# Optimization experiments

Measured on AMD Instinct MI355X. Metric: run time of the kernel, lower is better.

The kernel has to match this reference:

```python
import jax, jax.numpy as jnp
import numpy as np

C = 256          # in_channels
CI = 128         # inter_channels = C // reduction
N_B, H, W = 4, 64, 64


def setup_inputs() -> dict:
    key = jax.random.key(0)
    ks = jax.random.split(key, 9)
    std = 0.01
    inp = {
        "x": jax.random.normal(ks[0], (N_B, C, H, W), dtype=jnp.float32),
        # 1x1 conv weights stored as [out_ch, in_ch]
        "w_g": jax.random.normal(ks[1], (CI, C), dtype=jnp.float32) * std,
        "b_g": jnp.zeros((CI,), dtype=jnp.float32),
        "w_theta": jax.random.normal(ks[2], (CI, C), dtype=jnp.float32) * std,
        "b_theta": jnp.zeros((CI,), dtype=jnp.float32),
        "w_phi": jax.random.normal(ks[3], (CI, C), dtype=jnp.float32) * std,
        "b_phi": jnp.zeros((CI,), dtype=jnp.float32),
        # conv_out: use small random instead of exact zeros so output is non-trivial
        "w_out": jax.random.normal(ks[4], (C, CI), dtype=jnp.float32) * std,
        "b_out": jnp.zeros((C,), dtype=jnp.float32),
    }
    return inp


def reference(x, w_g, b_g, w_theta, b_theta, w_phi, b_phi, w_out, b_out):
    n, c, h, w = x.shape
    nhw = h * w
    xf = x.reshape(n, c, nhw)                                   # [n, C, N]
    # 1x1 convs == channel matmuls
    g_x = jnp.einsum('ncs,oc->nso', xf, w_g) + b_g              # [n, N, CI]
    theta_x = jnp.einsum('ncs,oc->nso', xf, w_theta) + b_theta  # [n, N, CI]
    phi_x = jnp.einsum('ncs,oc->nos', xf, w_phi) + b_phi[None, :, None]  # [n, CI, N]
    # pairwise weights: [n, N, N]
    pw = jnp.einsum('nqc,ncs->nqs', theta_x, phi_x)
    # faithful to original: DIVIDE by d**-0.5 (i.e. multiply by sqrt(d))
    pw = pw / (theta_x.shape[-1] ** (-0.5))
    pw = jax.nn.softmax(pw, axis=-1)
    y = jnp.einsum('nqs,nsc->nqc', pw, g_x)                     # [n, N, CI]
    y = y.transpose(0, 2, 1).reshape(n, -1, h, w)               # [n, CI, H, W]
    out = jnp.einsum('nchw,oc->nohw', y, w_out) + b_out[None, :, None, None]
    return x + out
```

## Files before the change

### kernel.cpp

```cpp
#include <hip/hip_runtime.h>
#include <cmath>

typedef __attribute__((ext_vector_type(8))) short bf16x8;
typedef __attribute__((ext_vector_type(4))) float f32x4;
typedef __attribute__((ext_vector_type(16))) float f32x16;

#define MFMA16(a,b,c)  __builtin_amdgcn_mfma_f32_16x16x32_bf16((a),(b),(c),0,0,0)
#define MFMA32(a,b,c)  __builtin_amdgcn_mfma_f32_32x32x16_bf16((a),(b),(c),0,0,0)

#if __has_builtin(__builtin_amdgcn_exp2f)
#define EXP2F(x) __builtin_amdgcn_exp2f(x)
#else
#define EXP2F(x) exp2f(x)
#endif

#define KSCALE 16.3222312f

#define NB 4
#define CH 256
#define CI 128
#define NS 4096

__device__ __forceinline__ unsigned short f2bf(float f) {
    unsigned int u = __builtin_bit_cast(unsigned int, f);
    u += 0x7fffu + ((u >> 16) & 1u);
    return (unsigned short)(u >> 16);
}
__device__ __forceinline__ unsigned int pk2(float lo, float hi) {
    return (unsigned int)f2bf(lo) | ((unsigned int)f2bf(hi) << 16);
}
__device__ __forceinline__ unsigned int pkt(float lo, float hi) {
    return __builtin_amdgcn_perm(__builtin_bit_cast(unsigned int, hi),
                                 __builtin_bit_cast(unsigned int, lo), 0x07060302u);
}
__device__ __forceinline__ float bf2f(unsigned int ush) {
    return __builtin_bit_cast(float, ush << 16);
}

__device__ __forceinline__ void plswap(unsigned int& wLow, unsigned int& wHigh) {
    asm volatile("v_permlane32_swap_b32 %0, %1" : "+v"(wLow), "+v"(wHigh));
}

__device__ __forceinline__ f32x16 zero16() {
    f32x16 v;
#pragma unroll
    for (int i = 0; i < 16; i++) v[i] = 0.f;
    return v;
}

__device__ __forceinline__ void gload16(void* lds, const void* g) {
    __builtin_amdgcn_global_load_lds(
        (const __attribute__((address_space(1))) unsigned int*)g,
        (__attribute__((address_space(3))) unsigned int*)lds,
        16, 0, 0);
}

__global__ void wcvt_kernel(const float* __restrict__ w_g, const float* __restrict__ w_th,
                            const float* __restrict__ w_ph, const float* __restrict__ w_out,
                            const float* __restrict__ b_g, const float* __restrict__ b_th,
                            const float* __restrict__ b_ph,
                            unsigned short* __restrict__ wbf, float* __restrict__ bsc) {
    int i = blockIdx.x * 256 + threadIdx.x;
    float v;
    if (i < 98304) {
        int wi = i >> 15;
        int r  = i & 32767;
        int oh = r >> 14;
        int r2 = r & 16383;
        int kc = r2 >> 11;
        int r3 = r2 & 2047;
        int ot = r3 >> 9;
        int r4 = r3 & 511;
        int lane = r4 >> 3;
        int e  = r4 & 7;
        int o = oh * 64 + ot * 16 + (lane & 15);
        int c = kc * 32 + (lane >> 4) * 8 + e;
        const float* W = (wi == 0) ? w_g : (wi == 1 ? w_th : w_ph);
        v = W[o * CH + c];
        if (wi == 1) v *= KSCALE;
    } else {
        int r = i - 98304;
        int oh = r >> 14;
        int r2 = r & 16383;
        int kc = r2 >> 12;
        int r3 = r2 & 4095;
        int ot = r3 >> 9;
        int r4 = r3 & 511;
        int lane = r4 >> 3;
        int e = r4 & 7;
        int o = oh * 128 + ot * 16 + (lane & 15);
        int c = kc * 32 + (lane >> 4) * 8 + e;
        v = w_out[o * CI + c];
    }
    wbf[i] = f2bf(v);
    if (i < 128)          bsc[i] = b_g[i];
    else if (i < 256)     bsc[i] = b_th[i - 128] * KSCALE;
    else if (i < 384)     bsc[i] = b_ph[i - 256];
}

__global__ __launch_bounds__(512, 2)
void proj_kernel(const float* __restrict__ x,
                 const unsigned short* __restrict__ wbf, const float* __restrict__ bsc,
                 unsigned short* __restrict__ theta,
                 unsigned short* __restrict__ phi,
                 unsigned short* __restrict__ gT) {
    const int tid  = threadIdx.x;
    const int wid  = tid >> 6;
    const int lane = tid & 63;
    const int quad = lane >> 4;
    const int l15  = lane & 15;
    const int stile = blockIdx.x;
    const int n     = blockIdx.y;
    const int s0    = stile * 64;

    const float* xN = x + (size_t)n * CH * NS;

    __shared__ unsigned int xp[64 * 128];

#pragma unroll
    for (int i = 0; i < 4; i++) {
        int t  = i * 512 + tid;
        int s4 = t & 15;
        int cp = t >> 4;
        const float* p0 = xN + (size_t)(2 * cp) * NS + s0 + s4 * 4;
        float4 a = *(const float4*)p0;
        float4 b = *(const float4*)(p0 + NS);
        int col = (((cp >> 2) ^ (s4 & 7)) << 2) | (cp & 3);
        unsigned int* xr = xp + (s4 * 4) * 128 + col;
        xr[0]   = pk2(a.x, b.x);
        xr[128] = pk2(a.y, b.y);
        xr[256] = pk2(a.z, b.z);
        xr[384] = pk2(a.w, b.w);
    }
    __syncthreads();

    const int srow = (wid & 3) * 16 + l15;
    const int oh   = wid >> 2;
    const int sw7  = (srow >> 2) & 7;
#pragma unroll
    for (int wi = 0; wi < 3; wi++) {
        f32x4 acc[4];
#pragma unroll
        for (int ot = 0; ot < 4; ot++) acc[ot] = (f32x4){0.f, 0.f, 0.f, 0.f};
        const unsigned short* W = wbf + (size_t)(wi * 2 + oh) * 16384;
#pragma unroll
        for (int kc = 0; kc < 8; kc++) {
            bf16x8 af = *(const bf16x8*)(&xp[srow * 128 + (((kc * 4 + quad) ^ sw7) << 2)]);
#pragma unroll
            for (int ot = 0; ot < 4; ot++) {
                bf16x8 wf = *(const bf16x8*)(W + kc * 2048 + ot * 512 + lane * 8);
                if (wi == 0) acc[ot] = MFMA16(af, wf, acc[ot]);
                else         acc[ot] = MFMA16(wf, af, acc[ot]);
            }
        }
        const float* Bv = bsc + wi * 128 + oh * 64;
        if (wi == 0) {
#pragma unroll
            for (int ot = 0; ot < 4; ot++) {
                int o = oh * 64 + ot * 16 + l15;
                float bias = Bv[ot * 16 + l15];
                int sg0 = s0 + (wid & 3) * 16 + quad * 4;
                uint2 w;
                w.x = pk2(acc[ot][0] + bias, acc[ot][1] + bias);
                w.y = pk2(acc[ot][2] + bias, acc[ot][3] + bias);
                *(uint2*)(gT + (size_t)((size_t)n * CI + o) * NS + sg0) = w;
            }
        } else {
            unsigned short* dst = (wi == 1) ? theta : phi;
            const int sgl = s0 + srow;
#pragma unroll
            for (int ot = 0; ot < 4; ot++) {
                f32x4 bb = *(const f32x4*)(Bv + ot * 16 + quad * 4);
                uint2 w;
                w.x = pk2(acc[ot][0] + bb[0], acc[ot][1] + bb[1]);
                w.y = pk2(acc[ot][2] + bb[2], acc[ot][3] + bb[3]);
                *(uint2*)(dst + ((size_t)n * NS + sgl) * CI + oh * 64 + ot * 16 + quad * 4) = w;
            }
        }
    }
}

__global__ __launch_bounds__(256, 2)
void attn_kernel(const unsigned short* __restrict__ theta,
                 const unsigned short* __restrict__ phi,
                 const unsigned short* __restrict__ gT,
                 unsigned short* __restrict__ Opart,
                 float* __restrict__ lbuf) {
    const int tid  = threadIdx.x;
    const int wid  = tid >> 6;
    const int lane = tid & 63;
    const int l31  = lane & 31;
    const int lh32 = lane >> 5;
    const int sn    = blockIdx.x;
    const int split = sn >> 2;
    const int n     = sn & 3;
    const int qb    = blockIdx.y;
    const int qbase = qb * 128 + wid * 32;

    const unsigned short* thN = theta + (size_t)n * NS * CI;
    const unsigned short* phN = phi   + (size_t)n * NS * CI;
    const unsigned short* gN  = gT    + (size_t)n * CI * NS;

    __shared__ unsigned short smem[32768];
    unsigned short* Kb = smem;
    unsigned short* Vb = smem + 16384;

    bf16x8 qf[8];
#pragma unroll
    for (int kc = 0; kc < 8; kc++)
        qf[kc] = *(const bf16x8*)(thN + (size_t)(qbase + l31) * CI + kc * 16 + lh32 * 8);

    f32x16 O[4];
#pragma unroll
    for (int ct = 0; ct < 4; ct++) O[ct] = zero16();
    float lrun = 0.f;

    const int sbase0 = split * 1024;
    const int lh16 = lane >> 4, lm16 = lane & 15;
    const int lh8  = lane >> 3, lm8  = lane & 7;

#pragma unroll
    for (int i = 0; i < 4; i++) {
        int seg = wid * 4 + i;
        int s   = seg * 4 + lh16;
        int j   = lm16 ^ (s & 15);
        gload16(Kb + seg * 512, phN + (size_t)(sbase0 + s) * CI + j * 8);
    }
#pragma unroll
    for (int i = 0; i < 4; i++) {
        int seg = wid * 4 + i;
        int c   = seg * 8 + lh8;
        int j   = lm8 ^ (c & 7);
        gload16(Vb + seg * 512, gN + (size_t)c * NS + sbase0 + j * 8);
    }

    for (int ck = 0; ck < 16; ck++) {
        const int cur = ck & 1, nxt = cur ^ 1;
        unsigned short* Kc = Kb + cur * 8192;
        unsigned short* Vc = Vb + cur * 8192;
        __syncthreads();

        if (ck + 1 < 16) {
            const int sb1 = sbase0 + (ck + 1) * 64;
#pragma unroll
            for (int i = 0; i < 4; i++) {
                int seg = wid * 4 + i;
                int s   = seg * 4 + lh16;
                int j   = lm16 ^ (s & 15);
                gload16(Kb + nxt * 8192 + seg * 512, phN + (size_t)(sb1 + s) * CI + j * 8);
            }
#pragma unroll
            for (int i = 0; i < 4; i++) {
                int seg = wid * 4 + i;
                int c   = seg * 8 + lh8;
                int j   = lm8 ^ (c & 7);
                gload16(Vb + nxt * 8192 + seg * 512, gN + (size_t)c * NS + sb1 + j * 8);
            }
        }

        f32x16 S[2];
        S[0] = zero16(); S[1] = zero16();
        __builtin_amdgcn_s_setprio(1);
#pragma unroll
        for (int sb = 0; sb < 2; sb++) {
#pragma unroll
            for (int kc = 0; kc < 8; kc++) {
                int s = sb * 32 + l31;
                bf16x8 kf = *(const bf16x8*)(Kc + s * 128 + (((kc * 2 + lh32) ^ (s & 15)) * 8));
                S[sb] = MFMA32(kf, qf[kc], S[sb]);
            }
        }
        __builtin_amdgcn_s_setprio(0);

        bf16x8 pf[4];
        float lsum = 0.f;
#pragma unroll
        for (int ks = 0; ks < 4; ks++) {
            const int sb = ks >> 1, b = ks & 1;
            float pA[4], pB[4];
#pragma unroll
            for (int m = 0; m < 4; m++) {
                pA[m] = EXP2F(S[sb][(2 * b) * 4 + m]);
                pB[m] = EXP2F(S[sb][(2 * b + 1) * 4 + m]);
            }
            lsum += ((pA[0] + pA[1]) + (pA[2] + pA[3]))
                  + ((pB[0] + pB[1]) + (pB[2] + pB[3]));
            unsigned int wA0 = pkt(pA[0], pA[1]);
            unsigned int wA1 = pkt(pA[2], pA[3]);
            unsigned int wB0 = pkt(pB[0], pB[1]);
            unsigned int wB1 = pkt(pB[2], pB[3]);
            plswap(wA0, wB0);
            plswap(wA1, wB1);
            union { unsigned int u[4]; bf16x8 v; } P;
            P.u[0] = wA0; P.u[1] = wA1; P.u[2] = wB0; P.u[3] = wB1;
            pf[ks] = P.v;
        }
        lrun += lsum;

        __builtin_amdgcn_s_setprio(1);
#pragma unroll
        for (int ks = 0; ks < 4; ks++) {
#pragma unroll
            for (int ct = 0; ct < 4; ct++) {
                int c = ct * 32 + l31;
                bf16x8 vf = *(const bf16x8*)(Vc + c * 64 + (((ks * 2 + lh32) ^ (c & 7)) * 8));
                O[ct] = MFMA32(vf, pf[ks], O[ct]);
            }
        }
        __builtin_amdgcn_s_setprio(0);
    }

    __syncthreads();
    float* tb = (float*)smem + wid * 2048;
    const size_t obase = ((size_t)(split * NB + n)) * NS * CI;
#pragma unroll
    for (int pass = 0; pass < 2; pass++) {
#pragma unroll
        for (int cti = 0; cti < 2; cti++) {
            const int ct = pass * 2 + cti;
#pragma unroll
            for (int g = 0; g < 4; g++) {
                const int c_local = cti * 32 + 8 * g + 4 * lh32;
                const int slot = (c_local >> 2) ^ (l31 & 15);
                f32x4 v;
                v[0] = O[ct][4 * g + 0]; v[1] = O[ct][4 * g + 1];
                v[2] = O[ct][4 * g + 2]; v[3] = O[ct][4 * g + 3];
                *(f32x4*)(tb + l31 * 64 + slot * 4) = v;
            }
        }
#pragma unroll
        for (int i = 0; i < 8; i++) {
            const int qr  = i * 4 + (lane >> 4);
            const int lin = lane & 15;
            f32x4 v = *(const f32x4*)(tb + qr * 64 + ((lin ^ (qr & 15)) * 4));
            uint2 w;
            w.x = pk2(v[0], v[1]);
            w.y = pk2(v[2], v[3]);
            *(uint2*)(Opart + obase + (size_t)(qbase + qr) * CI + pass * 64 + lin * 4) = w;
        }
    }
    lrun += __shfl_xor(lrun, 32);
    if (lane < 32)
        lbuf[(split * NB + n) * NS + qbase + l31] = lrun;
}

__global__ __launch_bounds__(256, 2)
void outproj_kernel(const float* __restrict__ x,
                    const unsigned short* __restrict__ wbf,
                    const float* __restrict__ b_out,
                    const unsigned short* __restrict__ Opart,
                    const float* __restrict__ lbuf,
                    float* __restrict__ out) {
    const int tid  = threadIdx.x;
    const int wid  = tid >> 6;
    const int lane = tid & 63;
    const int quad = lane >> 4;
    const int l15  = lane & 15;
    const int oh = blockIdx.y;
    const int n  = blockIdx.z;
    const int s0 = blockIdx.x * 64;
    const int sw = s0 + wid * 16;
    const int T  = NB * NS;

    __shared__ unsigned short Ob[4 * 64 * 128];

    const int lh16 = lane >> 4, lm16 = lane & 15;
#pragma unroll
    for (int k = 0; k < 4; k++) {
#pragma unroll
        for (int i = 0; i < 4; i++) {
            int seg = wid * 4 + i;
            int s   = seg * 4 + lh16;
            int j   = lm16 ^ (s & 15);
            gload16(Ob + k * 8192 + seg * 512,
                    Opart + ((size_t)k * T + (size_t)n * NS + s0 + s) * CI + j * 8);
        }
    }

    const int srow = n * NS + sw + l15;
    float l = 0.f;
#pragma unroll
    for (int k = 0; k < 4; k++) l += lbuf[k * T + srow];
    float rinv = 1.0f / l;

    __syncthreads();

    const int sL = wid * 16 + l15;
    bf16x8 yb[4];
#pragma unroll
    for (int kc = 0; kc < 4; kc++) {
        float f0 = 0.f, f1 = 0.f, f2 = 0.f, f3 = 0.f;
        float f4 = 0.f, f5 = 0.f, f6 = 0.f, f7 = 0.f;
        const int slot = (kc * 4 + quad) ^ (sL & 15);
#pragma unroll
        for (int k = 0; k < 4; k++) {
            uint4 v = *(const uint4*)(Ob + k * 8192 + sL * 128 + slot * 8);
            f0 += bf2f(v.x & 0xffffu); f1 += bf2f(v.x >> 16);
            f2 += bf2f(v.y & 0xffffu); f3 += bf2f(v.y >> 16);
            f4 += bf2f(v.z & 0xffffu); f5 += bf2f(v.z >> 16);
            f6 += bf2f(v.w & 0xffffu); f7 += bf2f(v.w >> 16);
        }
        union { unsigned int uu[4]; bf16x8 vv; } r;
        r.uu[0] = pk2(f0 * rinv, f1 * rinv);
        r.uu[1] = pk2(f2 * rinv, f3 * rinv);
        r.uu[2] = pk2(f4 * rinv, f5 * rinv);
        r.uu[3] = pk2(f6 * rinv, f7 * rinv);
        yb[kc] = r.vv;
    }

    const unsigned short* wof = wbf + 98304 + (size_t)oh * 16384;
    f32x4 acc[8];
#pragma unroll
    for (int ot = 0; ot < 8; ot++) acc[ot] = (f32x4){0.f, 0.f, 0.f, 0.f};
#pragma unroll
    for (int kc = 0; kc < 4; kc++) {
#pragma unroll
        for (int ot = 0; ot < 8; ot++) {
            bf16x8 wa = *(const bf16x8*)(wof + kc * 4096 + ot * 512 + lane * 8);
            acc[ot] = MFMA16(wa, yb[kc], acc[ot]);
        }
    }
#pragma unroll
    for (int ot = 0; ot < 8; ot++) {
#pragma unroll
        for (int r = 0; r < 4; r++) {
            int o = oh * 128 + ot * 16 + quad * 4 + r;
            size_t idx = ((size_t)n * CH + o) * NS + sw + l15;
            out[idx] = x[idx] + acc[ot][r] + b_out[o];
        }
    }
}

extern "C" void kernel_launch(void* const* d_in, const int* in_sizes, int n_in,
                              void* d_out, int out_size, void* d_ws, size_t ws_size,
                              hipStream_t stream) {
    const float* x     = (const float*)d_in[0];
    const float* w_g   = (const float*)d_in[1];
    const float* b_g   = (const float*)d_in[2];
    const float* w_th  = (const float*)d_in[3];
    const float* b_th  = (const float*)d_in[4];
    const float* w_ph  = (const float*)d_in[5];
    const float* b_ph  = (const float*)d_in[6];
    const float* w_out = (const float*)d_in[7];
    const float* b_out = (const float*)d_in[8];
    float* out = (float*)d_out;

    char* ws = (char*)d_ws;
    unsigned short* theta = (unsigned short*)(ws + 0);
    unsigned short* phi   = (unsigned short*)(ws + 4194304);
    unsigned short* gT    = (unsigned short*)(ws + 8388608);
    unsigned short* Opart = (unsigned short*)(ws + 12582912);
    float* lbuf  = (float*)(ws + 29360128);
    unsigned short* wbf = (unsigned short*)(ws + 29622272);
    float* bsc   = (float*)(ws + 29884416);

    wcvt_kernel<<<512, 256, 0, stream>>>(w_g, w_th, w_ph, w_out, b_g, b_th, b_ph, wbf, bsc);
    proj_kernel<<<dim3(64, NB), 512, 0, stream>>>(x, wbf, bsc, theta, phi, gT);
    attn_kernel<<<dim3(16, 32), 256, 0, stream>>>(theta, phi, gT, Opart, lbuf);
    outproj_kernel<<<dim3(64, 2, NB), 256, 0, stream>>>(x, wbf, b_out, Opart, lbuf, out);
}
```

Baseline: 146.7 us.

## Fuse four kernels into one cooperative persistent kernel with grid syncs

Merges the weight conversion, projection, attention and output projection kernels into a single cooperative launch of 256 blocks of 512 threads, separated by grid-wide barriers. Each block maps its work onto the old grids (two attention query tiles per block, both output halves per block). The output stage now reads the partial attention results straight from global memory instead of staging them in LDS. This removes three kernel launch gaps, at the cost of grid.sync overhead, possibly lower occupancy in the attention phase, and uncoalesced Opart reads.

```diff
diff --git a/kernel.cpp b/kernel.cpp
--- a/kernel.cpp
+++ b/kernel.cpp
@@ -1,5 +1,8 @@
 #include <hip/hip_runtime.h>
+#include <hip/hip_cooperative_groups.h>
 #include <cmath>
+
+namespace cg = cooperative_groups;
 
 typedef __attribute__((ext_vector_type(8))) short bf16x8;
 typedef __attribute__((ext_vector_type(4))) float f32x4;
@@ -55,378 +58,359 @@
         16, 0, 0);
 }
 
-__global__ void wcvt_kernel(const float* __restrict__ w_g, const float* __restrict__ w_th,
-                            const float* __restrict__ w_ph, const float* __restrict__ w_out,
-                            const float* __restrict__ b_g, const float* __restrict__ b_th,
-                            const float* __restrict__ b_ph,
-                            unsigned short* __restrict__ wbf, float* __restrict__ bsc) {
-    int i = blockIdx.x * 256 + threadIdx.x;
-    float v;
-    if (i < 98304) {
-        int wi = i >> 15;
-        int r  = i & 32767;
-        int oh = r >> 14;
-        int r2 = r & 16383;
-        int kc = r2 >> 11;
-        int r3 = r2 & 2047;
-        int ot = r3 >> 9;
-        int r4 = r3 & 511;
-        int lane = r4 >> 3;
-        int e  = r4 & 7;
-        int o = oh * 64 + ot * 16 + (lane & 15);
-        int c = kc * 32 + (lane >> 4) * 8 + e;
-        const float* W = (wi == 0) ? w_g : (wi == 1 ? w_th : w_ph);
-        v = W[o * CH + c];
-        if (wi == 1) v *= KSCALE;
-    } else {
-        int r = i - 98304;
-        int oh = r >> 14;
-        int r2 = r & 16383;
-        int kc = r2 >> 12;
-        int r3 = r2 & 4095;
-        int ot = r3 >> 9;
-        int r4 = r3 & 511;
-        int lane = r4 >> 3;
-        int e = r4 & 7;
-        int o = oh * 128 + ot * 16 + (lane & 15);
-        int c = kc * 32 + (lane >> 4) * 8 + e;
-        v = w_out[o * CI + c];
-    }
-    wbf[i] = f2bf(v);
-    if (i < 128)          bsc[i] = b_g[i];
-    else if (i < 256)     bsc[i] = b_th[i - 128] * KSCALE;
-    else if (i < 384)     bsc[i] = b_ph[i - 256];
-}
-
 __global__ __launch_bounds__(512, 2)
-void proj_kernel(const float* __restrict__ x,
-                 const unsigned short* __restrict__ wbf, const float* __restrict__ bsc,
-                 unsigned short* __restrict__ theta,
-                 unsigned short* __restrict__ phi,
-                 unsigned short* __restrict__ gT) {
+void fused_kernel(const float* __restrict__ x,
+                  const float* __restrict__ w_g,  const float* __restrict__ b_g,
+                  const float* __restrict__ w_th, const float* __restrict__ b_th,
+                  const float* __restrict__ w_ph, const float* __restrict__ b_ph,
+                  const float* __restrict__ w_out, const float* __restrict__ b_out,
+                  float* __restrict__ out,
+                  unsigned short* __restrict__ theta, unsigned short* __restrict__ phi,
+                  unsigned short* __restrict__ gT,
+                  unsigned short* __restrict__ Opart, float* __restrict__ lbuf,
+                  unsigned short* __restrict__ wbf, float* __restrict__ bsc) {
+    cg::grid_group grid = cg::this_grid();
     const int tid  = threadIdx.x;
+    const int bx   = blockIdx.x;
     const int wid  = tid >> 6;
     const int lane = tid & 63;
     const int quad = lane >> 4;
     const int l15  = lane & 15;
-    const int stile = blockIdx.x;
-    const int n     = blockIdx.y;
-    const int s0    = stile * 64;
-
-    const float* xN = x + (size_t)n * CH * NS;
-
-    __shared__ unsigned int xp[64 * 128];
-
-#pragma unroll
-    for (int i = 0; i < 4; i++) {
-        int t  = i * 512 + tid;
-        int s4 = t & 15;
-        int cp = t >> 4;
-        const float* p0 = xN + (size_t)(2 * cp) * NS + s0 + s4 * 4;
-        float4 a = *(const float4*)p0;
-        float4 b = *(const float4*)(p0 + NS);
-        int col = (((cp >> 2) ^ (s4 & 7)) << 2) | (cp & 3);
-        unsigned int* xr = xp + (s4 * 4) * 128 + col;
-        xr[0]   = pk2(a.x, b.x);
-        xr[128] = pk2(a.y, b.y);
-        xr[256] = pk2(a.z, b.z);
-        xr[384] = pk2(a.w, b.w);
+
+    __shared__ unsigned short smem[32768];
+
+    {
+        int i = bx * 512 + tid;
+        float v;
+        if (i < 98304) {
+            int wi = i >> 15;
+            int r  = i & 32767;
+            int oh = r >> 14;
+            int r2 = r & 16383;
+            int kc = r2 >> 11;
+            int r3 = r2 & 2047;
+            int ot = r3 >> 9;
+            int r4 = r3 & 511;
+            int ln = r4 >> 3;
+            int e  = r4 & 7;
+            int o = oh * 64 + ot * 16 + (ln & 15);
+            int c = kc * 32 + (ln >> 4) * 8 + e;
+            const float* W = (wi == 0) ? w_g : (wi == 1 ? w_th : w_ph);
+            v = W[o * CH + c];
+            if (wi == 1) v *= KSCALE;
+        } else {
+            int r = i - 98304;
+            int oh = r >> 14;
+            int r2 = r & 16383;
+            int kc = r2 >> 12;
+            int r3 = r2 & 4095;
+            int ot = r3 >> 9;
+            int r4 = r3 & 511;
+            int ln = r4 >> 3;
+            int e = r4 & 7;
+            int o = oh * 128 + ot * 16 + (ln & 15);
+            int c = kc * 32 + (ln >> 4) * 8 + e;
+            v = w_out[o * CI + c];
+        }
+        wbf[i] = f2bf(v);
+        if (i < 128)          bsc[i] = b_g[i];
+        else if (i < 256)     bsc[i] = b_th[i - 128] * KSCALE;
+        else if (i < 384)     bsc[i] = b_ph[i - 256];
     }
-    __syncthreads();
-
-    const int srow = (wid & 3) * 16 + l15;
-    const int oh   = wid >> 2;
-    const int sw7  = (srow >> 2) & 7;
-#pragma unroll
-    for (int wi = 0; wi < 3; wi++) {
-        f32x4 acc[4];
-#pragma unroll
-        for (int ot = 0; ot < 4; ot++) acc[ot] = (f32x4){0.f, 0.f, 0.f, 0.f};
-        const unsigned short* W = wbf + (size_t)(wi * 2 + oh) * 16384;
-#pragma unroll
-        for (int kc = 0; kc < 8; kc++) {
-            bf16x8 af = *(const bf16x8*)(&xp[srow * 128 + (((kc * 4 + quad) ^ sw7) << 2)]);
-#pragma unroll
-            for (int ot = 0; ot < 4; ot++) {
-                bf16x8 wf = *(const bf16x8*)(W + kc * 2048 + ot * 512 + lane * 8);
-                if (wi == 0) acc[ot] = MFMA16(af, wf, acc[ot]);
-                else         acc[ot] = MFMA16(wf, af, acc[ot]);
-            }
-        }
-        const float* Bv = bsc + wi * 128 + oh * 64;
-        if (wi == 0) {
-#pragma unroll
-            for (int ot = 0; ot < 4; ot++) {
-                int o = oh * 64 + ot * 16 + l15;
-                float bias = Bv[ot * 16 + l15];
-                int sg0 = s0 + (wid & 3) * 16 + quad * 4;
-                uint2 w;
-                w.x = pk2(acc[ot][0] + bias, acc[ot][1] + bias);
-                w.y = pk2(acc[ot][2] + bias, acc[ot][3] + bias);
-                *(uint2*)(gT + (size_t)((size_t)n * CI + o) * NS + sg0) = w;
-            }
-        } else {
-            unsigned short* dst = (wi == 1) ? theta : phi;
-            const int sgl = s0 + srow;
-#pragma unroll
-            for (int ot = 0; ot < 4; ot++) {
-                f32x4 bb = *(const f32x4*)(Bv + ot * 16 + quad * 4);
-                uint2 w;
-                w.x = pk2(acc[ot][0] + bb[0], acc[ot][1] + bb[1]);
-                w.y = pk2(acc[ot][2] + bb[2], acc[ot][3] + bb[3]);
-                *(uint2*)(dst + ((size_t)n * NS + sgl) * CI + oh * 64 + ot * 16 + quad * 4) = w;
+    __threadfence();
+    grid.sync();
+
+    {
+        const int stile = bx & 63;
+        const int n     = bx >> 6;
+        const int s0    = stile * 64;
+        const float* xN = x + (size_t)n * CH * NS;
+        unsigned int* xp = (unsigned int*)smem;
+
+#pragma unroll
+        for (int i = 0; i < 4; i++) {
+            int t  = i * 512 + tid;
+            int s4 = t & 15;
+            int cp = t >> 4;
+            const float* p0 = xN + (size_t)(2 * cp) * NS + s0 + s4 * 4;
+            float4 a = *(const float4*)p0;
+            float4 b = *(const float4*)(p0 + NS);
+            int col = (((cp >> 2) ^ (s4 & 7)) << 2) | (cp & 3);
+            unsigned int* xr = xp + (s4 * 4) * 128 + col;
+            xr[0]   = pk2(a.x, b.x);
+            xr[128] = pk2(a.y, b.y);
+            xr[256] = pk2(a.z, b.z);
+            xr[384] = pk2(a.w, b.w);
+        }
+        __syncthreads();
+
+        const int srow = (wid & 3) * 16 + l15;
+        const int oh   = wid >> 2;
+        const int sw7  = (srow >> 2) & 7;
+#pragma unroll
+        for (int wi = 0; wi < 3; wi++) {
+            f32x4 acc[4];
+#pragma unroll
+            for (int ot = 0; ot < 4; ot++) acc[ot] = (f32x4){0.f, 0.f, 0.f, 0.f};
+            const unsigned short* W = wbf + (size_t)(wi * 2 + oh) * 16384;
+#pragma unroll
+            for (int kc = 0; kc < 8; kc++) {
+                bf16x8 af = *(const bf16x8*)(&xp[srow * 128 + (((kc * 4 + quad) ^ sw7) << 2)]);
+#pragma unroll
+                for (int ot = 0; ot < 4; ot++) {
+                    bf16x8 wf = *(const bf16x8*)(W + kc * 2048 + ot * 512 + lane * 8);
+                    if (wi == 0) acc[ot] = MFMA16(af, wf, acc[ot]);
+                    else         acc[ot] = MFMA16(wf, af, acc[ot]);
+                }
+            }
+            const float* Bv = bsc + wi * 128 + oh * 64;
+            if (wi == 0) {
+#pragma unroll
+                for (int ot = 0; ot < 4; ot++) {
+                    int o = oh * 64 + ot * 16 + l15;
+                    float bias = Bv[ot * 16 + l15];
+                    int sg0 = s0 + (wid & 3) * 16 + quad * 4;
+                    uint2 w;
+                    w.x = pk2(acc[ot][0] + bias, acc[ot][1] + bias);
+                    w.y = pk2(acc[ot][2] + bias, acc[ot][3] + bias);
+                    *(uint2*)(gT + (size_t)((size_t)n * CI + o) * NS + sg0) = w;
+                }
+            } else {
+                unsigned short* dst = (wi == 1) ? theta : phi;
+                const int sgl = s0 + srow;
+#pragma unroll
+                for (int ot = 0; ot < 4; ot++) {
+                    f32x4 bb = *(const f32x4*)(Bv + ot * 16 + quad * 4);
+                    uint2 w;
+                    w.x = pk2(acc[ot][0] + bb[0], acc[ot][1] + bb[1]);
+                    w.y = pk2(acc[ot][2] + bb[2], acc[ot][3] + bb[3]);
+                    *(uint2*)(dst + ((size_t)n * NS + sgl) * CI + oh * 64 + ot * 16 + quad * 4) = w;
+                }
             }
         }
     }
-}
-
-__global__ __launch_bounds__(256, 2)
-void attn_kernel(const unsigned short* __restrict__ theta,
-                 const unsigned short* __restrict__ phi,
-                 const unsigned short* __restrict__ gT,
-                 unsigned short* __restrict__ Opart,
-                 float* __restrict__ lbuf) {
-    const int tid  = threadIdx.x;
-    const int wid  = tid >> 6;
-    const int lane = tid & 63;
-    const int l31  = lane & 31;
-    const int lh32 = lane >> 5;
-    const int sn    = blockIdx.x;
-    const int split = sn >> 2;
-    const int n     = sn & 3;
-    const int qb    = blockIdx.y;
-    const int qbase = qb * 128 + wid * 32;
-
-    const unsigned short* thN = theta + (size_t)n * NS * CI;
-    const unsigned short* phN = phi   + (size_t)n * NS * CI;
-    const unsigned short* gN  = gT    + (size_t)n * CI * NS;
-
-    __shared__ unsigned short smem[32768];
-    unsigned short* Kb = smem;
-    unsigned short* Vb = smem + 16384;
-
-    bf16x8 qf[8];
-#pragma unroll
-    for (int kc = 0; kc < 8; kc++)
-        qf[kc] = *(const bf16x8*)(thN + (size_t)(qbase + l31) * CI + kc * 16 + lh32 * 8);
-
-    f32x16 O[4];
-#pragma unroll
-    for (int ct = 0; ct < 4; ct++) O[ct] = zero16();
-    float lrun = 0.f;
-
-    const int sbase0 = split * 1024;
-    const int lh16 = lane >> 4, lm16 = lane & 15;
-    const int lh8  = lane >> 3, lm8  = lane & 7;
-
-#pragma unroll
-    for (int i = 0; i < 4; i++) {
-        int seg = wid * 4 + i;
-        int s   = seg * 4 + lh16;
-        int j   = lm16 ^ (s & 15);
-        gload16(Kb + seg * 512, phN + (size_t)(sbase0 + s) * CI + j * 8);
-    }
-#pragma unroll
-    for (int i = 0; i < 4; i++) {
-        int seg = wid * 4 + i;
-        int c   = seg * 8 + lh8;
-        int j   = lm8 ^ (c & 7);
-        gload16(Vb + seg * 512, gN + (size_t)c * NS + sbase0 + j * 8);
-    }
-
-    for (int ck = 0; ck < 16; ck++) {
-        const int cur = ck & 1, nxt = cur ^ 1;
-        unsigned short* Kc = Kb + cur * 8192;
-        unsigned short* Vc = Vb + cur * 8192;
-        __syncthreads();
-
-        if (ck + 1 < 16) {
-            const int sb1 = sbase0 + (ck + 1) * 64;
-#pragma unroll
-            for (int i = 0; i < 4; i++) {
-                int seg = wid * 4 + i;
-                int s   = seg * 4 + lh16;
-                int j   = lm16 ^ (s & 15);
-                gload16(Kb + nxt * 8192 + seg * 512, phN + (size_t)(sb1 + s) * CI + j * 8);
-            }
-#pragma unroll
-            for (int i = 0; i < 4; i++) {
-                int seg = wid * 4 + i;
-                int c   = seg * 8 + lh8;
-                int j   = lm8 ^ (c & 7);
-                gload16(Vb + nxt * 8192 + seg * 512, gN + (size_t)c * NS + sb1 + j * 8);
-            }
-        }
-
-        f32x16 S[2];
-        S[0] = zero16(); S[1] = zero16();
-        __builtin_amdgcn_s_setprio(1);
-#pragma unroll
-        for (int sb = 0; sb < 2; sb++) {
-#pragma unroll
-            for (int kc = 0; kc < 8; kc++) {
-                int s = sb * 32 + l31;
-                bf16x8 kf = *(const bf16x8*)(Kc + s * 128 + (((kc * 2 + lh32) ^ (s & 15)) * 8));
-                S[sb] = MFMA32(kf, qf[kc], S[sb]);
-            }
-        }
-        __builtin_amdgcn_s_setprio(0);
-
-        bf16x8 pf[4];
-        float lsum = 0.f;
-#pragma unroll
-        for (int ks = 0; ks < 4; ks++) {
-            const int sb = ks >> 1, b = ks & 1;
-            float pA[4], pB[4];
-#pragma unroll
-            for (int m = 0; m < 4; m++) {
-                pA[m] = EXP2F(S[sb][(2 * b) * 4 + m]);
-                pB[m] = EXP2F(S[sb][(2 * b + 1) * 4 + m]);
-            }
-            lsum += ((pA[0] + pA[1]) + (pA[2] + pA[3]))
-                  + ((pB[0] + pB[1]) + (pB[2] + pB[3]));
-            unsigned int wA0 = pkt(pA[0], pA[1]);
-            unsigned int wA1 = pkt(pA[2], pA[3]);
-            unsigned int wB0 = pkt(pB[0], pB[1]);
-            unsigned int wB1 = pkt(pB[2], pB[3]);
-            plswap(wA0, wB0);
-            plswap(wA1, wB1);
-            union { unsigned int u[4]; bf16x8 v; } P;
-            P.u[0] = wA0; P.u[1] = wA1; P.u[2] = wB0; P.u[3] = wB1;
-            pf[ks] = P.v;
-        }
-        lrun += lsum;
-
-        __builtin_amdgcn_s_setprio(1);
-#pragma unroll
-        for (int ks = 0; ks < 4; ks++) {
-#pragma unroll
-            for (int ct = 0; ct < 4; ct++) {
-                int c = ct * 32 + l31;
-                bf16x8 vf = *(const bf16x8*)(Vc + c * 64 + (((ks * 2 + lh32) ^ (c & 7)) * 8));
-                O[ct] = MFMA32(vf, pf[ks], O[ct]);
-            }
-        }
-        __builtin_amdgcn_s_setprio(0);
-    }
-
-    __syncthreads();
-    float* tb = (float*)smem + wid * 2048;
-    const size_t obase = ((size_t)(split * NB + n)) * NS * CI;
-#pragma unroll
-    for (int pass = 0; pass < 2; pass++) {
-#pragma unroll
-        for (int cti = 0; cti < 2; cti++) {
-            const int ct = pass * 2 + cti;
-#pragma unroll
-            for (int g = 0; g < 4; g++) {
-                const int c_local = cti * 32 + 8 * g + 4 * lh32;
-                const int slot = (c_local >> 2) ^ (l31 & 15);
-                f32x4 v;
-                v[0] = O[ct][4 * g + 0]; v[1] = O[ct][4 * g + 1];
-                v[2] = O[ct][4 * g + 2]; v[3] = O[ct][4 * g + 3];
-                *(f32x4*)(tb + l31 * 64 + slot * 4) = v;
-            }
-        }
-#pragma unroll
-        for (int i = 0; i < 8; i++) {
-            const int qr  = i * 4 + (lane >> 4);
-            const int lin = lane & 15;
-            f32x4 v = *(const f32x4*)(tb + qr * 64 + ((lin ^ (qr & 15)) * 4));
-            uint2 w;
-            w.x = pk2(v[0], v[1]);
-            w.y = pk2(v[2], v[3]);
-            *(uint2*)(Opart + obase + (size_t)(qbase + qr) * CI + pass * 64 + lin * 4) = w;
-        }
-    }
-    lrun += __shfl_xor(lrun, 32);
-    if (lane < 32)
-        lbuf[(split * NB + n) * NS + qbase + l31] = lrun;
-}
-
-__global__ __launch_bounds__(256, 2)
-void outproj_kernel(const float* __restrict__ x,
-                    const unsigned short* __restrict__ wbf,
-                    const float* __restrict__ b_out,
-                    const unsigned short* __restrict__ Opart,
-                    const float* __restrict__ lbuf,
-                    float* __restrict__ out) {
-    const int tid  = threadIdx.x;
-    const int wid  = tid >> 6;
-    const int lane = tid & 63;
-    const int quad = lane >> 4;
-    const int l15  = lane & 15;
-    const int oh = blockIdx.y;
-    const int n  = blockIdx.z;
-    const int s0 = blockIdx.x * 64;
-    const int sw = s0 + wid * 16;
-    const int T  = NB * NS;
-
-    __shared__ unsigned short Ob[4 * 64 * 128];
-
-    const int lh16 = lane >> 4, lm16 = lane & 15;
-#pragma unroll
-    for (int k = 0; k < 4; k++) {
-#pragma unroll
-        for (int i = 0; i < 4; i++) {
-            int seg = wid * 4 + i;
+    __threadfence();
+    grid.sync();
+
+    {
+        const int l31  = lane & 31;
+        const int lh32 = lane >> 5;
+        const int sn    = bx & 15;
+        const int split = sn >> 2;
+        const int n     = sn & 3;
+        const int qb    = (bx >> 4) * 2 + (wid >> 2);
+        const int wv    = wid & 3;
+        const int qbase = qb * 128 + wv * 32;
+
+        const unsigned short* thN = theta + (size_t)n * NS * CI;
+        const unsigned short* phN = phi   + (size_t)n * NS * CI;
+        const unsigned short* gN  = gT    + (size_t)n * CI * NS;
+
+        unsigned short* Kb = smem;
+        unsigned short* Vb = smem + 16384;
+
+        bf16x8 qf[8];
+#pragma unroll
+        for (int kc = 0; kc < 8; kc++)
+            qf[kc] = *(const bf16x8*)(thN + (size_t)(qbase + l31) * CI + kc * 16 + lh32 * 8);
+
+        f32x16 O[4];
+#pragma unroll
+        for (int ct = 0; ct < 4; ct++) O[ct] = zero16();
+        float lrun = 0.f;
+
+        const int sbase0 = split * 1024;
+        const int lh16 = lane >> 4, lm16 = lane & 15;
+        const int lh8  = lane >> 3, lm8  = lane & 7;
+
+#pragma unroll
+        for (int i = 0; i < 2; i++) {
+            int seg = wid * 2 + i;
             int s   = seg * 4 + lh16;
             int j   = lm16 ^ (s & 15);
-            gload16(Ob + k * 8192 + seg * 512,
-                    Opart + ((size_t)k * T + (size_t)n * NS + s0 + s) * CI + j * 8);
-        }
+            gload16(Kb + seg * 512, phN + (size_t)(sbase0 + s) * CI + j * 8);
+        }
+#pragma unroll
+        for (int i = 0; i < 2; i++) {
+            int seg = wid * 2 + i;
+            int c   = seg * 8 + lh8;
+            int j   = lm8 ^ (c & 7);
+            gload16(Vb + seg * 512, gN + (size_t)c * NS + sbase0 + j * 8);
+        }
+
+        for (int ck = 0; ck < 16; ck++) {
+            const int cur = ck & 1, nxt = cur ^ 1;
+            unsigned short* Kc = Kb + cur * 8192;
+            unsigned short* Vc = Vb + cur * 8192;
+            __syncthreads();
+
+            if (ck + 1 < 16) {
+                const int sb1 = sbase0 + (ck + 1) * 64;
+#pragma unroll
+                for (int i = 0; i < 2; i++) {
+                    int seg = wid * 2 + i;
+                    int s   = seg * 4 + lh16;
+                    int j   = lm16 ^ (s & 15);
+                    gload16(Kb + nxt * 8192 + seg * 512, phN + (size_t)(sb1 + s) * CI + j * 8);
+                }
+#pragma unroll
+                for (int i = 0; i < 2; i++) {
+                    int seg = wid * 2 + i;
+                    int c   = seg * 8 + lh8;
+                    int j   = lm8 ^ (c & 7);
+                    gload16(Vb + nxt * 8192 + seg * 512, gN + (size_t)c * NS + sb1 + j * 8);
+                }
+            }
+
+            f32x16 S[2];
+            S[0] = zero16(); S[1] = zero16();
+            __builtin_amdgcn_s_setprio(1);
+#pragma unroll
+            for (int sb = 0; sb < 2; sb++) {
+#pragma unroll
+                for (int kc = 0; kc < 8; kc++) {
+                    int s = sb * 32 + l31;
+                    bf16x8 kf = *(const bf16x8*)(Kc + s * 128 + (((kc * 2 + lh32) ^ (s & 15)) * 8));
+                    S[sb] = MFMA32(kf, qf[kc], S[sb]);
+                }
+            }
+            __builtin_amdgcn_s_setprio(0);
+
+            bf16x8 pf[4];
+            float lsum = 0.f;
+#pragma unroll
+            for (int ks = 0; ks < 4; ks++) {
+                const int sb = ks >> 1, b = ks & 1;
+                float pA[4], pB[4];
+#pragma unroll
+                for (int m = 0; m < 4; m++) {
+                    pA[m] = EXP2F(S[sb][(2 * b) * 4 + m]);
+                    pB[m] = EXP2F(S[sb][(2 * b + 1) * 4 + m]);
+                }
+                lsum += ((pA[0] + pA[1]) + (pA[2] + pA[3]))
+                      + ((pB[0] + pB[1]) + (pB[2] + pB[3]));
+                unsigned int wA0 = pkt(pA[0], pA[1]);
+                unsigned int wA1 = pkt(pA[2], pA[3]);
+                unsigned int wB0 = pkt(pB[0], pB[1]);
+                unsigned int wB1 = pkt(pB[2], pB[3]);
+                plswap(wA0, wB0);
+                plswap(wA1, wB1);
+                union { unsigned int u[4]; bf16x8 v; } P;
+                P.u[0] = wA0; P.u[1] = wA1; P.u[2] = wB0; P.u[3] = wB1;
+                pf[ks] = P.v;
+            }
+            lrun += lsum;
+
+            __builtin_amdgcn_s_setprio(1);
+#pragma unroll
+            for (int ks = 0; ks < 4; ks++) {
+#pragma unroll
+                for (int ct = 0; ct < 4; ct++) {
+                    int c = ct * 32 + l31;
+                    bf16x8 vf = *(const bf16x8*)(Vc + c * 64 + (((ks * 2 + lh32) ^ (c & 7)) * 8));
+                    O[ct] = MFMA32(vf, pf[ks], O[ct]);
+                }
+            }
+            __builtin_amdgcn_s_setprio(0);
+        }
+
+        __syncthreads();
+        float* tb = (float*)smem + wid * 2048;
+        const size_t obase = ((size_t)(split * NB + n)) * NS * CI;
+#pragma unroll
+        for (int pass = 0; pass < 2; pass++) {
+#pragma unroll
+            for (int cti = 0; cti < 2; cti++) {
+                const int ct = pass * 2 + cti;
+#pragma unroll
+                for (int g = 0; g < 4; g++) {
+                    const int c_local = cti * 32 + 8 * g + 4 * lh32;
+                    const int slot = (c_local >> 2) ^ (l31 & 15);
+                    f32x4 v;
+                    v[0] = O[ct][4 * g + 0]; v[1] = O[ct][4 * g + 1];
+                    v[2] = O[ct][4 * g + 2]; v[3] = O[ct][4 * g + 3];
+                    *(f32x4*)(tb + l31 * 64 + slot * 4) = v;
+                }
+            }
+#pragma unroll
+            for (int i = 0; i < 8; i++) {
+                const int qr  = i * 4 + (lane >> 4);
+                const int lin = lane & 15;
+                f32x4 v = *(const f32x4*)(tb + qr * 64 + ((lin ^ (qr & 15)) * 4));
+                uint2 w;
+                w.x = pk2(v[0], v[1]);
+                w.y = pk2(v[2], v[3]);
+                *(uint2*)(Opart + obase + (size_t)(qbase + qr) * CI + pass * 64 + lin * 4) = w;
+            }
+        }
+        lrun += __shfl_xor(lrun, 32);
+        if (lane < 32)
+            lbuf[(split * NB + n) * NS + qbase + l31] = lrun;
     }
-
-    const int srow = n * NS + sw + l15;
-    float l = 0.f;
-#pragma unroll
-    for (int k = 0; k < 4; k++) l += lbuf[k * T + srow];
-    float rinv = 1.0f / l;
-
-    __syncthreads();
-
-    const int sL = wid * 16 + l15;
-    bf16x8 yb[4];
-#pragma unroll
-    for (int kc = 0; kc < 4; kc++) {
-        float f0 = 0.f, f1 = 0.f, f2 = 0.f, f3 = 0.f;
-        float f4 = 0.f, f5 = 0.f, f6 = 0.f, f7 = 0.f;
-        const int slot = (kc * 4 + quad) ^ (sL & 15);
-#pragma unroll
-        for (int k = 0; k < 4; k++) {
-            uint4 v = *(const uint4*)(Ob + k * 8192 + sL * 128 + slot * 8);
-            f0 += bf2f(v.x & 0xffffu); f1 += bf2f(v.x >> 16);
-            f2 += bf2f(v.y & 0xffffu); f3 += bf2f(v.y >> 16);
-            f4 += bf2f(v.z & 0xffffu); f5 += bf2f(v.z >> 16);
-            f6 += bf2f(v.w & 0xffffu); f7 += bf2f(v.w >> 16);
-        }
-        union { unsigned int uu[4]; bf16x8 vv; } r;
-        r.uu[0] = pk2(f0 * rinv, f1 * rinv);
-        r.uu[1] = pk2(f2 * rinv, f3 * rinv);
-        r.uu[2] = pk2(f4 * rinv, f5 * rinv);
-        r.uu[3] = pk2(f6 * rinv, f7 * rinv);
-        yb[kc] = r.vv;
-    }
-
-    const unsigned short* wof = wbf + 98304 + (size_t)oh * 16384;
-    f32x4 acc[8];
-#pragma unroll
-    for (int ot = 0; ot < 8; ot++) acc[ot] = (f32x4){0.f, 0.f, 0.f, 0.f};
-#pragma unroll
-    for (int kc = 0; kc < 4; kc++) {
-#pragma unroll
-        for (int ot = 0; ot < 8; ot++) {
-            bf16x8 wa = *(const bf16x8*)(wof + kc * 4096 + ot * 512 + lane * 8);
-            acc[ot] = MFMA16(wa, yb[kc], acc[ot]);
-        }
-    }
-#pragma unroll
-    for (int ot = 0; ot < 8; ot++) {
-#pragma unroll
-        for (int r = 0; r < 4; r++) {
-            int o = oh * 128 + ot * 16 + quad * 4 + r;
-            size_t idx = ((size_t)n * CH + o) * NS + sw + l15;
-            out[idx] = x[idx] + acc[ot][r] + b_out[o];
+    __threadfence();
+    grid.sync();
+
+    {
+        const int stile = bx & 63;
+        const int n     = bx >> 6;
+        const int s0    = stile * 64;
+        const int swq   = wid & 3;
+        const int oth   = wid >> 2;
+        const int sw    = s0 + swq * 16;
+        const int T     = NB * NS;
+
+        const int srow = n * NS + sw + l15;
+        float l = 0.f;
+#pragma unroll
+        for (int k = 0; k < 4; k++) l += lbuf[k * T + srow];
+        float rinv = 1.0f / l;
+
+        bf16x8 yb[4];
+#pragma unroll
+        for (int kc = 0; kc < 4; kc++) {
+            float f0 = 0.f, f1 = 0.f, f2 = 0.f, f3 = 0.f;
+            float f4 = 0.f, f5 = 0.f, f6 = 0.f, f7 = 0.f;
+#pragma unroll
+            for (int k = 0; k < 4; k++) {
+                uint4 v = *(const uint4*)(Opart + ((size_t)k * T + srow) * CI + kc * 32 + quad * 8);
+                f0 += bf2f(v.x & 0xffffu); f1 += bf2f(v.x >> 16);
+                f2 += bf2f(v.y & 0xffffu); f3 += bf2f(v.y >> 16);
+                f4 += bf2f(v.z & 0xffffu); f5 += bf2f(v.z >> 16);
+                f6 += bf2f(v.w & 0xffffu); f7 += bf2f(v.w >> 16);
+            }
+            union { unsigned int uu[4]; bf16x8 vv; } r;
+            r.uu[0] = pk2(f0 * rinv, f1 * rinv);
+            r.uu[1] = pk2(f2 * rinv, f3 * rinv);
+            r.uu[2] = pk2(f4 * rinv, f5 * rinv);
+            r.uu[3] = pk2(f6 * rinv, f7 * rinv);
+            yb[kc] = r.vv;
+        }
+
+#pragma unroll
+        for (int oh = 0; oh < 2; oh++) {
+            const unsigned short* wof = wbf + 98304 + (size_t)oh * 16384;
+            f32x4 acc[4];
+#pragma unroll
+            for (int oi = 0; oi < 4; oi++) acc[oi] = (f32x4){0.f, 0.f, 0.f, 0.f};
+#pragma unroll
+            for (int kc = 0; kc < 4; kc++) {
+#pragma unroll
+                for (int oi = 0; oi < 4; oi++) {
+                    int ot = oth * 4 + oi;
+                    bf16x8 wa = *(const bf16x8*)(wof + kc * 4096 + ot * 512 + lane * 8);
+                    acc[oi] = MFMA16(wa, yb[kc], acc[oi]);
+                }
+            }
+#pragma unroll
+            for (int oi = 0; oi < 4; oi++) {
+                int ot = oth * 4 + oi;
+#pragma unroll
+                for (int r = 0; r < 4; r++) {
+                    int o = oh * 128 + ot * 16 + quad * 4 + r;
+                    size_t idx = ((size_t)n * CH + o) * NS + sw + l15;
+                    out[idx] = x[idx] + acc[oi][r] + b_out[o];
+                }
+            }
         }
     }
 }
@@ -454,8 +438,10 @@
     unsigned short* wbf = (unsigned short*)(ws + 29622272);
     float* bsc   = (float*)(ws + 29884416);
 
-    wcvt_kernel<<<512, 256, 0, stream>>>(w_g, w_th, w_ph, w_out, b_g, b_th, b_ph, wbf, bsc);
-    proj_kernel<<<dim3(64, NB), 512, 0, stream>>>(x, wbf, bsc, theta, phi, gT);
-    attn_kernel<<<dim3(16, 32), 256, 0, stream>>>(theta, phi, gT, Opart, lbuf);
-    outproj_kernel<<<dim3(64, 2, NB), 256, 0, stream>>>(x, wbf, b_out, Opart, lbuf, out);
-}
+    void* args[] = { (void*)&x, (void*)&w_g, (void*)&b_g, (void*)&w_th, (void*)&b_th,
+                     (void*)&w_ph, (void*)&b_ph, (void*)&w_out, (void*)&b_out,
+                     (void*)&out, (void*)&theta, (void*)&phi, (void*)&gT,
+                     (void*)&Opart, (void*)&lbuf, (void*)&wbf, (void*)&bsc };
+    hipLaunchCooperativeKernel((const void*)fused_kernel, dim3(256), dim3(512),
+                               args, 0, stream);
+}
```

Result: slower. 397.5 us (+170.9%).
